# Performance work log

Hardware: AMD Instinct MI355X
Metric: run time of the kernel (lower is better)

Reference implementation:

```python
import jax, jax.numpy as jnp
import numpy as np
from jax import lax

N_NODES = 10000
N_EDGES = 320000


def setup_inputs() -> dict:
    key = jax.random.key(0)
    ks = jax.random.split(key, 7)
    B, H, N, F = 4, 24, N_NODES, 32
    hid = 64
    x = jax.random.normal(ks[0], (B, H, N, F), dtype=jnp.float32)
    mask = jax.random.uniform(ks[1], (B, H), dtype=jnp.float32)
    edge_index = jax.random.randint(ks[2], (2, N_EDGES), 0, N, dtype=jnp.int32)
    W1 = jax.random.normal(ks[3], (F + 1, hid), dtype=jnp.float32) * (1.0 / np.sqrt(F + 1))
    b1 = jax.random.normal(ks[4], (hid,), dtype=jnp.float32) * 0.02
    W2 = jax.random.normal(ks[5], (hid, F), dtype=jnp.float32) * (1.0 / np.sqrt(hid))
    b2 = jax.random.normal(ks[6], (F,), dtype=jnp.float32) * 0.02
    return {"x": x, "mask": mask, "edge_index": edge_index,
            "W1": W1, "b1": b1, "W2": W2, "b2": b2}


def _gcn_norm(edge_index, num_nodes):
    # PyG GCNConv default: add self loops, symmetric normalization.
    loops = jnp.arange(num_nodes, dtype=edge_index.dtype)
    src = jnp.concatenate([edge_index[0], loops])
    dst = jnp.concatenate([edge_index[1], loops])
    deg = jax.ops.segment_sum(jnp.ones_like(dst, dtype=jnp.float32), dst,
                              num_segments=num_nodes)
    dinv = jnp.where(deg > 0, lax.rsqrt(jnp.maximum(deg, 1e-12)), 0.0)
    norm = dinv[src] * dinv[dst]  # [E']
    return src, dst, norm


def reference(x, mask, edge_index, W1, b1, W2, b2):
    B, H, N, F = x.shape
    src, dst, norm = _gcn_norm(edge_index, N)

    def gcn(h, W, b):
        # h: [B, N, Fin] -> lin, then normalized neighbor aggregation, then bias
        hw = h @ W                                   # [B, N, Fout]
        msg = hw[:, src, :].transpose(1, 0, 2)       # [E', B, Fout]
        msg = msg * norm[:, None, None]
        agg = jax.ops.segment_sum(msg, dst, num_segments=N)  # [N, B, Fout]
        return agg.transpose(1, 0, 2) + b

    def per_hour(carry, inp):
        xh, mh = inp                                 # xh: [B, N, F], mh: [B]
        mc = jnp.broadcast_to(mh[:, None, None], (B, N, 1))
        h = jnp.concatenate([xh, mc], axis=-1)       # [B, N, F+1]
        out = jnp.tanh(gcn(gcn(h, W1, b1), W2, b2))  # [B, N, F]
        return carry, out

    _, outs = lax.scan(per_hour, None,
                       (x.transpose(1, 0, 2, 3), mask.T))  # [H, B, N, F]
    return outs.transpose(1, 0, 2, 3)                     # [B, H, N, F]
```

## Files before the change

### kernel.cpp

```cpp
#include <hip/hip_runtime.h>
#include <hip/hip_fp16.h>

#define NN 10000
#define FF 32
#define PG 4
#define NGRP 24

__device__ __forceinline__ unsigned short f2h(float f){
  union { unsigned short s; _Float16 h; } c; c.h = (_Float16)f; return c.s;
}

__device__ __forceinline__ void fmix2(float& ax, float& ay, float w, unsigned h){
  asm("v_fma_mix_f32 %0, %2, %3, %0 op_sel_hi:[0,1,0]\n\t"
      "v_fma_mix_f32 %1, %2, %3, %1 op_sel:[0,1,0] op_sel_hi:[0,1,0]"
      : "+v"(ax), "+v"(ay) : "v"(w), "v"(h));
}

__global__ void k_count(const int* __restrict__ dst, int* __restrict__ cnt, int E){
  int e = blockIdx.x * 256 + threadIdx.x;
  if (e < E) atomicAdd(&cnt[dst[e]], 1);
}

__global__ __launch_bounds__(1024) void k_scan(const int* __restrict__ cnt,
                                               int* __restrict__ off,
                                               float* __restrict__ dinv,
                                               const float* __restrict__ W1,
                                               const float* __restrict__ W2,
                                               const float* __restrict__ b1,
                                               float* __restrict__ W12,
                                               float* __restrict__ bb){
  __shared__ int wsum[16];
  __shared__ int carry;
  int tid = threadIdx.x, lane = tid & 63, wv = tid >> 6;
  if (tid == 0) carry = 0;
  __syncthreads();
  for (int base = 0; base < NN; base += 1024){
    int i = base + tid;
    int c = (i < NN) ? cnt[i] : 0;
    int v = (c + 3) & ~3;
    int s = v;
    #pragma unroll
    for (int o = 1; o < 64; o <<= 1){
      int t = __shfl_up(s, o, 64);
      if (lane >= o) s += t;
    }
    if (lane == 63) wsum[wv] = s;
    __syncthreads();
    if (tid == 0){
      int a = carry;
      #pragma unroll
      for (int k = 0; k < 16; ++k){ int t = wsum[k]; wsum[k] = a; a += t; }
      carry = a;
    }
    __syncthreads();
    if (i < NN){
      off[i]  = wsum[wv] + s - v;
      dinv[i] = rsqrtf((float)(c + 1));
    }
    __syncthreads();
  }
  if (tid == 0) off[NN] = carry;
  for (int idx = tid; idx < 33 * 32; idx += 1024){
    int k = idx >> 5, j = idx & 31;
    float s = 0.f;
    for (int m = 0; m < 64; ++m) s += W1[k * 64 + m] * W2[m * 32 + j];
    W12[idx] = s;
  }
  if (tid < 32){
    int j = tid;
    float s = 0.f;
    for (int m = 0; m < 64; ++m) s += b1[m] * W2[m * 32 + j];
    bb[j] = s;
  }
}

__global__ void k_scatter(const int* __restrict__ ei, const int* __restrict__ off,
                          int* __restrict__ cur, const float* __restrict__ dinv,
                          int2* __restrict__ csr, int E){
  int e = blockIdx.x * 256 + threadIdx.x;
  if (e >= E) return;
  int s = ei[e], d = ei[E + e];
  int pos = off[d] + atomicAdd(&cur[d], 1);
  csr[pos] = make_int2(s << 8, __float_as_int(dinv[s]));
}

__global__ void k_srow(const int* __restrict__ off, const int2* __restrict__ csr,
                       const float* __restrict__ dinv, float* __restrict__ srow){
  int n = blockIdx.x * 256 + threadIdx.x;
  if (n >= NN) return;
  float a = dinv[n];
  int e0 = off[n], e1 = off[n + 1];
  for (int j = e0; j < e1; ++j) a += __int_as_float(csr[j].y);
  srow[n] = dinv[n] * a;
}

__global__ __launch_bounds__(256) void k_gemm1(const float* __restrict__ x,
    const float* __restrict__ mask, const float* __restrict__ W12,
    unsigned* __restrict__ hw){
  const int pg = blockIdx.y;
  const int n  = blockIdx.x * 256 + threadIdx.x;
  const int grp = pg >> 2, p = pg & 3;
  const float mv = mask[pg];
  float acc[32];
  #pragma unroll
  for (int f = 0; f < 32; ++f) acc[f] = mv * W12[32 * 32 + f];
  if (n >= NN) return;
  const float4* xp = (const float4*)(x + (size_t)pg * (NN * FF) + (size_t)n * FF);
  float xv[32];
  #pragma unroll
  for (int i = 0; i < 8; ++i){
    float4 v = xp[i];
    xv[4*i]   = v.x; xv[4*i+1] = v.y;
    xv[4*i+2] = v.z; xv[4*i+3] = v.w;
  }
  #pragma unroll
  for (int k = 0; k < 32; ++k){
    const float xk = xv[k];
    #pragma unroll
    for (int f = 0; f < 32; ++f) acc[f] += xk * W12[k * 32 + f];
  }
  unsigned* hwg = hw + (size_t)grp * (NN * 64) + ((size_t)n << 6) + (p << 4);
  #pragma unroll
  for (int j = 0; j < 4; ++j){
    uint4 u;
    u.x = (unsigned)f2h(acc[8*j+0]) | ((unsigned)f2h(acc[8*j+1]) << 16);
    u.y = (unsigned)f2h(acc[8*j+2]) | ((unsigned)f2h(acc[8*j+3]) << 16);
    u.z = (unsigned)f2h(acc[8*j+4]) | ((unsigned)f2h(acc[8*j+5]) << 16);
    u.w = (unsigned)f2h(acc[8*j+6]) | ((unsigned)f2h(acc[8*j+7]) << 16);
    ((uint4*)hwg)[j] = u;
  }
}

__device__ __forceinline__ void map_block(int bx, int& grp, int& chunk){
  int r  = bx / 5000;
  int w8 = bx % 5000;
  grp   = r * 8 + (w8 & 7);
  chunk = w8 >> 3;
}

__device__ __forceinline__ void agg_edges(int e0, int e1,
    const int2* __restrict__ csr, const char* __restrict__ Vb, int loff,
    float& ax, float& ay){
  int nq = (e1 - e0) >> 2;
  if (nq <= 0) return;
  const int4* c4 = (const int4*)(csr + e0);
  const int qlast = nq - 1;
  int4 cA, dA, cB, dB, cC, dC, cD, dD;
  int4 cA2, dA2, cB2, dB2, cC2, dC2, cD2, dD2;
  unsigned rA0,rA1,rA2,rA3, rB0,rB1,rB2,rB3;
  unsigned rC0,rC1,rC2,rC3, rD0,rD1,rD2,rD3;
  {
    int i1 = 1<=qlast?1:qlast, i2 = 2<=qlast?2:qlast, i3 = 3<=qlast?3:qlast;
    cA = c4[0];      dA = c4[1];
    cB = c4[2*i1];   dB = c4[2*i1+1];
    cC = c4[2*i2];   dC = c4[2*i2+1];
    cD = c4[2*i3];   dD = c4[2*i3+1];
    int i4 = 4<=qlast?4:qlast, i5 = 5<=qlast?5:qlast;
    int i6 = 6<=qlast?6:qlast, i7 = 7<=qlast?7:qlast;
    cA2 = c4[2*i4];  dA2 = c4[2*i4+1];
    cB2 = c4[2*i5];  dB2 = c4[2*i5+1];
    cC2 = c4[2*i6];  dC2 = c4[2*i6+1];
    cD2 = c4[2*i7];  dD2 = c4[2*i7+1];
    rA0 = *(const unsigned*)(Vb + (unsigned)(cA.x + loff));
    rA1 = *(const unsigned*)(Vb + (unsigned)(cA.z + loff));
    rA2 = *(const unsigned*)(Vb + (unsigned)(dA.x + loff));
    rA3 = *(const unsigned*)(Vb + (unsigned)(dA.z + loff));
    rB0 = *(const unsigned*)(Vb + (unsigned)(cB.x + loff));
    rB1 = *(const unsigned*)(Vb + (unsigned)(cB.z + loff));
    rB2 = *(const unsigned*)(Vb + (unsigned)(dB.x + loff));
    rB3 = *(const unsigned*)(Vb + (unsigned)(dB.z + loff));
    rC0 = *(const unsigned*)(Vb + (unsigned)(cC.x + loff));
    rC1 = *(const unsigned*)(Vb + (unsigned)(cC.z + loff));
    rC2 = *(const unsigned*)(Vb + (unsigned)(dC.x + loff));
    rC3 = *(const unsigned*)(Vb + (unsigned)(dC.z + loff));
    rD0 = *(const unsigned*)(Vb + (unsigned)(cD.x + loff));
    rD1 = *(const unsigned*)(Vb + (unsigned)(cD.z + loff));
    rD2 = *(const unsigned*)(Vb + (unsigned)(dD.x + loff));
    rD3 = *(const unsigned*)(Vb + (unsigned)(dD.z + loff));
  }
  int q = 0;
  #define AGG_STEP(cX, dX, cX2, dX2, r0, r1, r2, r3, LEAD)              \
    do {                                                                \
      fmix2(ax, ay, __int_as_float(cX.y), r0);                          \
      fmix2(ax, ay, __int_as_float(cX.w), r1);                          \
      fmix2(ax, ay, __int_as_float(dX.y), r2);                          \
      fmix2(ax, ay, __int_as_float(dX.w), r3);                          \
      r0 = *(const unsigned*)(Vb + (unsigned)(cX2.x + loff));           \
      r1 = *(const unsigned*)(Vb + (unsigned)(cX2.z + loff));           \
      r2 = *(const unsigned*)(Vb + (unsigned)(dX2.x + loff));           \
      r3 = *(const unsigned*)(Vb + (unsigned)(dX2.z + loff));           \
      cX = cX2; dX = dX2;                                               \
      int ii = q + (LEAD); ii = ii <= qlast ? ii : qlast;               \
      cX2 = c4[2*ii]; dX2 = c4[2*ii+1];                                 \
    } while (0)
  for (; q + 3 < nq; q += 4){
    AGG_STEP(cA,dA,cA2,dA2, rA0,rA1,rA2,rA3, 8);
    AGG_STEP(cB,dB,cB2,dB2, rB0,rB1,rB2,rB3, 9);
    AGG_STEP(cC,dC,cC2,dC2, rC0,rC1,rC2,rC3, 10);
    AGG_STEP(cD,dD,cD2,dD2, rD0,rD1,rD2,rD3, 11);
  }
  #undef AGG_STEP
  int rem = nq - q;
  if (rem > 0){
    fmix2(ax, ay, __int_as_float(cA.y), rA0);
    fmix2(ax, ay, __int_as_float(cA.w), rA1);
    fmix2(ax, ay, __int_as_float(dA.y), rA2);
    fmix2(ax, ay, __int_as_float(dA.w), rA3);
  }
  if (rem > 1){
    fmix2(ax, ay, __int_as_float(cB.y), rB0);
    fmix2(ax, ay, __int_as_float(cB.w), rB1);
    fmix2(ax, ay, __int_as_float(dB.y), rB2);
    fmix2(ax, ay, __int_as_float(dB.w), rB3);
  }
  if (rem > 2){
    fmix2(ax, ay, __int_as_float(cC.y), rC0);
    fmix2(ax, ay, __int_as_float(cC.w), rC1);
    fmix2(ax, ay, __int_as_float(dC.y), rC2);
    fmix2(ax, ay, __int_as_float(dC.w), rC3);
  }
}

__global__ __launch_bounds__(256) void k_agg1(const int* __restrict__ off,
    const int2* __restrict__ csr, const float* __restrict__ dinv,
    const unsigned int* __restrict__ V, unsigned int* __restrict__ T){
  int grp, chunk; map_block(blockIdx.x, grp, chunk);
  int tid = threadIdx.x;
  int l = tid & 63;
  int wv = __builtin_amdgcn_readfirstlane(tid) >> 6;
  const char* Vb = (const char*)(V + (size_t)grp * (NN * 64));
  unsigned int* Tg = T + (size_t)grp * (NN * 64);
  int loff = l * 4;
  for (int it = 0; it < 4; ++it){
    int n = chunk * 16 + wv * 4 + it;
    float din = dinv[n];
    int e0 = off[n], e1 = off[n + 1];
    unsigned sv = *(const unsigned*)(Vb + (unsigned)((n << 8) + loff));
    float ax = 0.f, ay = 0.f;
    fmix2(ax, ay, din, sv);
    agg_edges(e0, e1, csr, Vb, loff, ax, ay);
    Tg[((size_t)n << 6) + l] =
        (unsigned)f2h(din * ax) | ((unsigned)f2h(din * ay) << 16);
  }
}

__global__ __launch_bounds__(256) void k_agg2(const int* __restrict__ off,
    const int2* __restrict__ csr, const float* __restrict__ dinv,
    const float* __restrict__ srow, const float* __restrict__ bb,
    const float* __restrict__ b2, const unsigned int* __restrict__ V,
    float* __restrict__ out){
  int grp, chunk; map_block(blockIdx.x, grp, chunk);
  int tid = threadIdx.x;
  int l = tid & 63;
  int wv = __builtin_amdgcn_readfirstlane(tid) >> 6;
  int p = l >> 4, fi = l & 15;
  const char* Vb = (const char*)(V + (size_t)grp * (NN * 64));
  int pg = grp * PG + p;
  float2 bbq = ((const float2*)bb)[fi];
  float2 b2q = ((const float2*)b2)[fi];
  float* outp = out + (size_t)pg * (NN * FF);
  int loff = l * 4;
  for (int it = 0; it < 4; ++it){
    int n = chunk * 16 + wv * 4 + it;
    float din = dinv[n];
    int e0 = off[n], e1 = off[n + 1];
    unsigned sv = *(const unsigned*)(Vb + (unsigned)((n << 8) + loff));
    float ax = 0.f, ay = 0.f;
    fmix2(ax, ay, din, sv);
    agg_edges(e0, e1, csr, Vb, loff, ax, ay);
    float sr = srow[n];
    float2 o;
    o.x = tanhf(din * ax + sr * bbq.x + b2q.x);
    o.y = tanhf(din * ay + sr * bbq.y + b2q.y);
    ((float2*)(outp + (size_t)n * FF))[fi] = o;
  }
}

extern "C" void kernel_launch(void* const* d_in, const int* in_sizes, int n_in,
                              void* d_out, int out_size, void* d_ws, size_t ws_size,
                              hipStream_t stream){
  const float* x    = (const float*)d_in[0];
  const float* mask = (const float*)d_in[1];
  const int*   ei   = (const int*)d_in[2];
  const float* W1   = (const float*)d_in[3];
  const float* b1   = (const float*)d_in[4];
  const float* W2   = (const float*)d_in[5];
  const float* b2   = (const float*)d_in[6];
  float* out = (float*)d_out;
  const int E = in_sizes[2] / 2;
  const int CSRCAP = E + 3 * NN + 64;

  char* wsp = (char*)d_ws;
  auto alloc = [&](size_t bytes) -> char* {
    char* p = wsp; wsp += (bytes + 255) & ~(size_t)255; return p;
  };
  int*   cnt  = (int*)  alloc((size_t)NN * 4);
  int*   off  = (int*)  alloc((size_t)(NN + 1) * 4);
  int*   cur  = (int*)  alloc((size_t)NN * 4);
  float* dinv = (float*)alloc((size_t)NN * 4);
  float* srow = (float*)alloc((size_t)NN * 4);
  float* W12  = (float*)alloc(33 * 32 * 4);
  float* bbv  = (float*)alloc(32 * 4);
  int2*  csr  = (int2*) alloc((size_t)CSRCAP * 8);
  const size_t per_group = (size_t)NN * 64 * 4;
  unsigned int* hw = (unsigned int*)alloc((size_t)NGRP * per_group);
  unsigned int* t1 = (unsigned int*)alloc((size_t)NGRP * per_group);

  hipMemsetAsync(cnt, 0, (size_t)NN * 4, stream);
  hipMemsetAsync(cur, 0, (size_t)NN * 4, stream);
  hipMemsetAsync(csr, 0, (size_t)CSRCAP * 8, stream);
  k_count  <<<(E + 255) / 256, 256, 0, stream>>>(ei + E, cnt, E);
  k_scan   <<<1, 1024, 0, stream>>>(cnt, off, dinv, W1, W2, b1, W12, bbv);
  k_scatter<<<(E + 255) / 256, 256, 0, stream>>>(ei, off, cur, dinv, csr, E);
  k_srow   <<<(NN + 255) / 256, 256, 0, stream>>>(off, csr, dinv, srow);

  k_gemm1<<<dim3(40, 96), 256, 0, stream>>>(x, mask, W12, hw);
  k_agg1 <<<15000, 256, 0, stream>>>(off, csr, dinv, hw, t1);
  k_agg2 <<<15000, 256, 0, stream>>>(off, csr, dinv, srow, bbv, b2, t1, out);
}
```

Before: 549.7 us.

## Fold memsets and srow kernel into count/scatter, use packed FMA in gemm

Zeroing the CSR buffer moves into k_count, and the separate cnt, cur and srow memsets merge into one contiguous memset. The srow kernel is removed: its neighbor sums are now built with float atomics during scatter and finished inside agg2. The gemm switches to v_pk_fma_f32 with W12 as scalar operands, and the self-loop term uses a plain f16 convert instead of fma_mix. Together these cut launch count and setup overhead, at the cost of atomic contention on srow and possible small floating-point ordering differences.

```diff
diff --git a/kernel.cpp b/kernel.cpp
--- a/kernel.cpp
+++ b/kernel.cpp
@@ -6,6 +6,8 @@
 #define PG 4
 #define NGRP 24
 
+typedef __attribute__((ext_vector_type(2))) float f32x2;
+
 __device__ __forceinline__ unsigned short f2h(float f){
   union { unsigned short s; _Float16 h; } c; c.h = (_Float16)f; return c.s;
 }
@@ -16,9 +18,18 @@
       : "+v"(ax), "+v"(ay) : "v"(w), "v"(h));
 }
 
-__global__ void k_count(const int* __restrict__ dst, int* __restrict__ cnt, int E){
+__device__ __forceinline__ void pkfma(f32x2& acc, f32x2 w, f32x2 x){
+  asm("v_pk_fma_f32 %0, %1, %2, %0" : "+v"(acc) : "s"(w), "v"(x));
+}
+
+__global__ void k_count(const int* __restrict__ dst, int* __restrict__ cnt,
+                        int2* __restrict__ csr, int csrcap, int E){
   int e = blockIdx.x * 256 + threadIdx.x;
-  if (e < E) atomicAdd(&cnt[dst[e]], 1);
+  if (e >= E) return;
+  csr[e] = make_int2(0, 0);
+  int e2 = e + E;
+  if (e2 < csrcap) csr[e2] = make_int2(0, 0);
+  atomicAdd(&cnt[dst[e]], 1);
 }
 
 __global__ __launch_bounds__(1024) void k_scan(const int* __restrict__ cnt,
@@ -76,22 +87,14 @@
 
 __global__ void k_scatter(const int* __restrict__ ei, const int* __restrict__ off,
                           int* __restrict__ cur, const float* __restrict__ dinv,
-                          int2* __restrict__ csr, int E){
+                          int2* __restrict__ csr, float* __restrict__ srow, int E){
   int e = blockIdx.x * 256 + threadIdx.x;
   if (e >= E) return;
   int s = ei[e], d = ei[E + e];
+  float ds = dinv[s];
   int pos = off[d] + atomicAdd(&cur[d], 1);
-  csr[pos] = make_int2(s << 8, __float_as_int(dinv[s]));
-}
-
-__global__ void k_srow(const int* __restrict__ off, const int2* __restrict__ csr,
-                       const float* __restrict__ dinv, float* __restrict__ srow){
-  int n = blockIdx.x * 256 + threadIdx.x;
-  if (n >= NN) return;
-  float a = dinv[n];
-  int e0 = off[n], e1 = off[n + 1];
-  for (int j = e0; j < e1; ++j) a += __int_as_float(csr[j].y);
-  srow[n] = dinv[n] * a;
+  csr[pos] = make_int2(s << 8, __float_as_int(ds));
+  atomicAdd(&srow[d], ds);
 }
 
 __global__ __launch_bounds__(256) void k_gemm1(const float* __restrict__ x,
@@ -101,9 +104,13 @@
   const int n  = blockIdx.x * 256 + threadIdx.x;
   const int grp = pg >> 2, p = pg & 3;
   const float mv = mask[pg];
-  float acc[32];
+  const f32x2* Wp = (const f32x2*)W12;
+  f32x2 acc[16];
   #pragma unroll
-  for (int f = 0; f < 32; ++f) acc[f] = mv * W12[32 * 32 + f];
+  for (int qf = 0; qf < 16; ++qf){
+    f32x2 w = Wp[32 * 16 + qf];
+    acc[qf].x = mv * w.x; acc[qf].y = mv * w.y;
+  }
   if (n >= NN) return;
   const float4* xp = (const float4*)(x + (size_t)pg * (NN * FF) + (size_t)n * FF);
   float xv[32];
@@ -115,18 +122,18 @@
   }
   #pragma unroll
   for (int k = 0; k < 32; ++k){
-    const float xk = xv[k];
+    f32x2 xk2; xk2.x = xv[k]; xk2.y = xv[k];
     #pragma unroll
-    for (int f = 0; f < 32; ++f) acc[f] += xk * W12[k * 32 + f];
+    for (int qf = 0; qf < 16; ++qf) pkfma(acc[qf], Wp[k * 16 + qf], xk2);
   }
   unsigned* hwg = hw + (size_t)grp * (NN * 64) + ((size_t)n << 6) + (p << 4);
   #pragma unroll
   for (int j = 0; j < 4; ++j){
     uint4 u;
-    u.x = (unsigned)f2h(acc[8*j+0]) | ((unsigned)f2h(acc[8*j+1]) << 16);
-    u.y = (unsigned)f2h(acc[8*j+2]) | ((unsigned)f2h(acc[8*j+3]) << 16);
-    u.z = (unsigned)f2h(acc[8*j+4]) | ((unsigned)f2h(acc[8*j+5]) << 16);
-    u.w = (unsigned)f2h(acc[8*j+6]) | ((unsigned)f2h(acc[8*j+7]) << 16);
+    u.x = (unsigned)f2h(acc[4*j+0].x) | ((unsigned)f2h(acc[4*j+0].y) << 16);
+    u.y = (unsigned)f2h(acc[4*j+1].x) | ((unsigned)f2h(acc[4*j+1].y) << 16);
+    u.z = (unsigned)f2h(acc[4*j+2].x) | ((unsigned)f2h(acc[4*j+2].y) << 16);
+    u.w = (unsigned)f2h(acc[4*j+3].x) | ((unsigned)f2h(acc[4*j+3].y) << 16);
     ((uint4*)hwg)[j] = u;
   }
 }
@@ -236,8 +243,9 @@
     float din = dinv[n];
     int e0 = off[n], e1 = off[n + 1];
     unsigned sv = *(const unsigned*)(Vb + (unsigned)((n << 8) + loff));
-    float ax = 0.f, ay = 0.f;
-    fmix2(ax, ay, din, sv);
+    union { unsigned u; _Float16 h[2]; } cv; cv.u = sv;
+    float ax = din * (float)cv.h[0];
+    float ay = din * (float)cv.h[1];
     agg_edges(e0, e1, csr, Vb, loff, ax, ay);
     Tg[((size_t)n << 6) + l] =
         (unsigned)f2h(din * ax) | ((unsigned)f2h(din * ay) << 16);
@@ -265,10 +273,11 @@
     float din = dinv[n];
     int e0 = off[n], e1 = off[n + 1];
     unsigned sv = *(const unsigned*)(Vb + (unsigned)((n << 8) + loff));
-    float ax = 0.f, ay = 0.f;
-    fmix2(ax, ay, din, sv);
+    union { unsigned u; _Float16 h[2]; } cv; cv.u = sv;
+    float ax = din * (float)cv.h[0];
+    float ay = din * (float)cv.h[1];
     agg_edges(e0, e1, csr, Vb, loff, ax, ay);
-    float sr = srow[n];
+    float sr = din * (din + srow[n]);
     float2 o;
     o.x = tanhf(din * ax + sr * bbq.x + b2q.x);
     o.y = tanhf(din * ay + sr * bbq.y + b2q.y);
@@ -297,8 +306,8 @@
   int*   cnt  = (int*)  alloc((size_t)NN * 4);
   int*   off  = (int*)  alloc((size_t)(NN + 1) * 4);
   int*   cur  = (int*)  alloc((size_t)NN * 4);
+  float* srow = (float*)alloc((size_t)NN * 4);
   float* dinv = (float*)alloc((size_t)NN * 4);
-  float* srow = (float*)alloc((size_t)NN * 4);
   float* W12  = (float*)alloc(33 * 32 * 4);
   float* bbv  = (float*)alloc(32 * 4);
   int2*  csr  = (int2*) alloc((size_t)CSRCAP * 8);
@@ -306,13 +315,11 @@
   unsigned int* hw = (unsigned int*)alloc((size_t)NGRP * per_group);
   unsigned int* t1 = (unsigned int*)alloc((size_t)NGRP * per_group);
 
-  hipMemsetAsync(cnt, 0, (size_t)NN * 4, stream);
-  hipMemsetAsync(cur, 0, (size_t)NN * 4, stream);
-  hipMemsetAsync(csr, 0, (size_t)CSRCAP * 8, stream);
-  k_count  <<<(E + 255) / 256, 256, 0, stream>>>(ei + E, cnt, E);
+  size_t zspan = (size_t)((char*)dinv - (char*)cnt);
+  hipMemsetAsync(cnt, 0, zspan, stream);
+  k_count  <<<(E + 255) / 256, 256, 0, stream>>>(ei + E, cnt, csr, CSRCAP, E);
   k_scan   <<<1, 1024, 0, stream>>>(cnt, off, dinv, W1, W2, b1, W12, bbv);
-  k_scatter<<<(E + 255) / 256, 256, 0, stream>>>(ei, off, cur, dinv, csr, E);
-  k_srow   <<<(NN + 255) / 256, 256, 0, stream>>>(off, csr, dinv, srow);
+  k_scatter<<<(E + 255) / 256, 256, 0, stream>>>(ei, off, cur, dinv, csr, srow, E);
 
   k_gemm1<<<dim3(40, 96), 256, 0, stream>>>(x, mask, W12, hw);
   k_agg1 <<<15000, 256, 0, stream>>>(off, csr, dinv, hw, t1);
```

Result: faster. 513.4 us (-6.6%).
